# Performance work log

Measured on AMD Instinct MI355X. Metric: run time of the kernel, lower is better.

The kernel has to match this reference:

```python
import jax, jax.numpy as jnp
import numpy as np
from jax.ops import segment_sum

N_NODES = 100000
N_EDGES = 1600000
N_GRAPHS = 128
HIDDEN = 128
N_CLASSES = 10


def setup_inputs() -> dict:
    key = jax.random.key(0)
    ks = jax.random.split(key, 8)
    src = jax.random.randint(ks[0], (N_EDGES,), 0, N_NODES, dtype=jnp.int32)
    dst = jax.random.randint(ks[1], (N_EDGES,), 0, N_NODES, dtype=jnp.int32)
    graph_ids = jnp.sort(jax.random.randint(ks[2], (N_NODES,), 0, N_GRAPHS, dtype=jnp.int32))
    W1 = jax.random.normal(ks[3], (1, HIDDEN), dtype=jnp.float32)
    b1 = jnp.zeros((HIDDEN,), jnp.float32)
    W2 = jax.random.normal(ks[4], (HIDDEN, HIDDEN), dtype=jnp.float32) * 0.05
    b2 = jnp.zeros((HIDDEN,), jnp.float32)
    Wc = jax.random.normal(ks[5], (HIDDEN, N_CLASSES), dtype=jnp.float32) * 0.05
    bc = jnp.zeros((N_CLASSES,), jnp.float32)
    return {"src": src, "dst": dst, "graph_ids": graph_ids,
            "W1": W1, "b1": b1, "W2": W2, "b2": b2, "Wc": Wc, "bc": bc}


def _graph_conv(h, src, dst, norm_src, norm_dst, W, b, n_nodes):
    # DGL GraphConv, norm='both': D_out^{-1/2} gather -> scatter-sum -> W -> D_in^{-1/2} -> +b
    hs = h * norm_src[:, None]
    agg = segment_sum(hs[src], dst, num_segments=n_nodes)  # [N, F_in]
    return agg @ W * norm_dst[:, None] + b


def reference(src, dst, graph_ids, W1, b1, W2, b2, Wc, bc):
    n_nodes = graph_ids.shape[0]
    ones_e = jnp.ones(src.shape[0], jnp.float32)
    indeg = segment_sum(ones_e, dst, num_segments=n_nodes)
    outdeg = segment_sum(ones_e, src, num_segments=n_nodes)
    norm_src = jnp.clip(outdeg, 1.0, None) ** -0.5
    norm_dst = jnp.clip(indeg, 1.0, None) ** -0.5

    h = indeg[:, None]  # node feature = in-degree, [N, 1]
    h = jax.nn.relu(_graph_conv(h, src, dst, norm_src, norm_dst, W1, b1, n_nodes))
    h = jax.nn.relu(_graph_conv(h, src, dst, norm_src, norm_dst, W2, b2, n_nodes))

    # dgl.mean_nodes: per-graph mean pooling
    sums = segment_sum(h, graph_ids, num_segments=N_GRAPHS)          # [G, H]
    cnts = segment_sum(jnp.ones(n_nodes, jnp.float32), graph_ids, num_segments=N_GRAPHS)
    hg = sums / jnp.clip(cnts, 1.0, None)[:, None]
    return hg @ Wc + bc  # [G, n_classes]
```

## Files before the change

kernel.cpp:

```cpp
#include <hip/hip_runtime.h>

#define N_NODES   100000
#define N_EDGES   1600000
#define N_GRAPHS  128
#define HIDDEN    128
#define N_CLASSES 10

#define BSH   9
#define BSZ   512
#define NBUCK 196
#define CAP   16384
#define PCH   4096
#define PTH   512
#define PIT   (PCH / PTH)

typedef unsigned int   uint;
typedef unsigned short ushort;
typedef unsigned char  uchar;

__global__ __launch_bounds__(PTH)
void k_part(const int* __restrict__ src, const int* __restrict__ dst,
            unsigned* __restrict__ bcur1, unsigned* __restrict__ bcur2,
            unsigned* __restrict__ tmp1, ushort* __restrict__ tmp2, int nE) {
    __shared__ unsigned hist[256], scanT[256], lcur[256], base[256];
    __shared__ unsigned stag4[PCH];
    __shared__ uchar    stagB[PCH];
    int t = threadIdx.x;
    int e0 = blockIdx.x * PCH;
    int e1 = min(e0 + PCH, nE);
    int cntE = e1 - e0;

    int sv[PIT], dv[PIT];
    if (t < 256) hist[t] = 0;
    __syncthreads();
    #pragma unroll
    for (int m = 0; m < PIT; ++m) {
        int e = e0 + t + m * PTH;
        if (e < e1) {
            sv[m] = src[e]; dv[m] = dst[e];
            atomicAdd(&hist[dv[m] >> BSH], 1u);
        }
    }
    __syncthreads();
    unsigned v = (t < 256) ? hist[t] : 0u;
    if (t < 256) scanT[t] = v;
    __syncthreads();
    for (int off = 1; off < 256; off <<= 1) {
        unsigned add = (t < 256 && t >= off) ? scanT[t - off] : 0u;
        __syncthreads();
        if (t < 256) scanT[t] += add;
        __syncthreads();
    }
    if (t < 256) {
        unsigned excl = scanT[t] - v;
        lcur[t] = excl;
        if (v > 0) { unsigned g = atomicAdd(&bcur1[t], v); base[t] = (unsigned)t * CAP + g - excl; }
    }
    __syncthreads();
    #pragma unroll
    for (int m = 0; m < PIT; ++m) {
        int e = e0 + t + m * PTH;
        if (e < e1) {
            int d = dv[m], s = sv[m];
            int b = d >> BSH;
            unsigned p = atomicAdd(&lcur[b], 1u);
            stag4[p] = ((unsigned)(d & (BSZ - 1)) << 17) | (unsigned)s;
            stagB[p] = (uchar)b;
        }
    }
    __syncthreads();
    for (int i = t; i < cntE; i += PTH) {
        unsigned b = stagB[i];
        unsigned a = base[b] + (unsigned)i;
        if (a < (b + 1u) * CAP) tmp1[a] = stag4[i];
    }
    __syncthreads();

    if (t < 256) hist[t] = 0;
    __syncthreads();
    #pragma unroll
    for (int m = 0; m < PIT; ++m) {
        int e = e0 + t + m * PTH;
        if (e < e1) atomicAdd(&hist[sv[m] >> BSH], 1u);
    }
    __syncthreads();
    v = (t < 256) ? hist[t] : 0u;
    if (t < 256) scanT[t] = v;
    __syncthreads();
    for (int off = 1; off < 256; off <<= 1) {
        unsigned add = (t < 256 && t >= off) ? scanT[t - off] : 0u;
        __syncthreads();
        if (t < 256) scanT[t] += add;
        __syncthreads();
    }
    if (t < 256) {
        unsigned excl = scanT[t] - v;
        lcur[t] = excl;
        if (v > 0) { unsigned g = atomicAdd(&bcur2[t], v); base[t] = (unsigned)t * CAP + g - excl; }
    }
    __syncthreads();
    ushort* st2 = (ushort*)stag4;
    #pragma unroll
    for (int m = 0; m < PIT; ++m) {
        int e = e0 + t + m * PTH;
        if (e < e1) {
            int s = sv[m];
            int b = s >> BSH;
            unsigned p = atomicAdd(&lcur[b], 1u);
            st2[p]   = (ushort)(s & (BSZ - 1));
            stagB[p] = (uchar)b;
        }
    }
    __syncthreads();
    for (int i = t; i < cntE; i += PTH) {
        unsigned b = stagB[i];
        unsigned a = base[b] + (unsigned)i;
        if (a < (b + 1u) * CAP) tmp2[a] = st2[i];
    }
}

__global__ __launch_bounds__(1024)
void k_ind_csr(const unsigned* __restrict__ bcur1, const unsigned* __restrict__ tmp1,
               const unsigned* __restrict__ bcur2, const ushort* __restrict__ tmp2,
               unsigned* __restrict__ indeg, float* __restrict__ ns,
               float* __restrict__ hs0, int* __restrict__ rs,
               int* __restrict__ csr) {
    __shared__ unsigned cin[BSZ], cout[BSZ], pref[BSZ], lcur[BSZ];
    int b = blockIdx.x, t = threadIdx.x;
    if (t < BSZ) { cin[t] = 0; cout[t] = 0; }
    __syncthreads();
    unsigned f1 = min(bcur1[b], (unsigned)CAP);
    const unsigned* tp1 = tmp1 + (size_t)b * CAP;
    for (unsigned i = t; i < f1; i += 1024) atomicAdd(&cin[tp1[i] >> 17], 1u);
    unsigned f2 = min(bcur2[b], (unsigned)CAP);
    const ushort* tp2 = tmp2 + (size_t)b * CAP;
    for (unsigned i = t; i < f2; i += 1024) atomicAdd(&cout[tp2[i]], 1u);
    __syncthreads();
    unsigned v = (t < BSZ) ? cin[t] : 0u;
    if (t < BSZ) pref[t] = v;
    __syncthreads();
    for (int off = 1; off < BSZ; off <<= 1) {
        unsigned add = (t < BSZ && t >= off) ? pref[t - off] : 0u;
        __syncthreads();
        if (t < BSZ) pref[t] += add;
        __syncthreads();
    }
    if (t < BSZ) {
        unsigned excl = pref[t] - v;
        lcur[t] = excl;
        int n = b * BSZ + t;
        if (n < N_NODES) {
            unsigned ci = cin[t], co = cout[t];
            float nsv = rsqrtf(fmaxf((float)co, 1.0f));
            indeg[n] = ci;
            ns[n]    = nsv;
            hs0[n]   = (float)ci * nsv;
            rs[n]    = (int)(b * CAP + excl);
        }
    }
    __syncthreads();
    int* cb = csr + (size_t)b * CAP;
    for (unsigned i = t; i < f1; i += 1024) {
        unsigned e = tp1[i];
        unsigned pos = atomicAdd(&lcur[e >> 17], 1u);
        cb[pos] = (int)(e & 0x1FFFFu);
    }
}

__global__ __launch_bounds__(256)
void k_conv1_info(const int* __restrict__ rs, const int* __restrict__ csr,
                  const float* __restrict__ hs0, const unsigned* __restrict__ indeg,
                  const float* __restrict__ ns,
                  const float* __restrict__ W1, const float* __restrict__ b1,
                  const float* __restrict__ W2,
                  float* __restrict__ U, float* __restrict__ V,
                  float4* __restrict__ info, int nN) {
    __shared__ float sts[128];
    int t = threadIdx.x;
    if (t < 128) {
        float w = W1[t], bb = b1[t];
        sts[t] = (w != 0.0f) ? (-bb / w) : 1e30f;
    }
    __syncthreads();
    for (int k = 2; k <= 128; k <<= 1) {
        for (int j = k >> 1; j > 0; j >>= 1) {
            if (t < 128) {
                int ixj = t ^ j;
                if (ixj > t) {
                    float a = sts[t], bb = sts[ixj];
                    bool up = ((t & k) == 0);
                    if (up ? (a > bb) : (a < bb)) { sts[t] = bb; sts[ixj] = a; }
                }
            }
            __syncthreads();
        }
    }
    if (blockIdx.x < 129 && t < 128) {
        int sg = blockIdx.x;
        float a_rep;
        if (sg == 0)        a_rep = sts[0]   - 1.0f;
        else if (sg == 128) a_rep = sts[127] + 1.0f;
        else                a_rep = 0.5f * (sts[sg - 1] + sts[sg]);
        float u = 0.0f, vv = 0.0f;
        for (int j = 0; j < 128; ++j) {
            float w = W1[j], bb = b1[j];
            if (a_rep * w + bb > 0.0f) {
                float w2 = W2[j * HIDDEN + t];
                u  += w * w2;
                vv += bb * w2;
            }
        }
        U[sg * HIDDEN + t] = u;
        V[sg * HIDDEN + t] = vv;
    }
    int node = blockIdx.x * 128 + (t >> 1);
    if (node >= nN) return;
    int j  = t & 1;
    int r0 = rs[node];
    int c  = (int)indeg[node];
    float a = 0.0f;
    #pragma unroll 4
    for (int k = j; k < c; k += 2) a += hs0[csr[r0 + k]];
    a += __shfl_xor(a, 1);
    float nd = rsqrtf(fmaxf((float)c, 1.0f));
    float av = a * nd;
    int sgp = 0;
    #pragma unroll
    for (int q = 0; q < 64; ++q) sgp += (sts[2 * q + j] < av) ? 1 : 0;
    sgp += __shfl_xor(sgp, 1);
    if (j == 0) {
        float nsv = ns[node];
        info[node] = make_float4(nsv * av, nsv, __int_as_float(sgp), nd);
    }
}

__global__ __launch_bounds__(256)
void k_conv2_pool(const int* __restrict__ rs, const int* __restrict__ csr,
                  const float4* __restrict__ info, const unsigned* __restrict__ indeg,
                  const float* __restrict__ U, const float* __restrict__ V,
                  const int* __restrict__ graph_ids, const float* __restrict__ b2,
                  float* __restrict__ pool, float* __restrict__ cnt, int nN) {
    __shared__ float sA[64], sB[64], sND[64];
    __shared__ int   sSg[64], sGr[64], sR[64], sC[64];
    int blockBase = blockIdx.x * 64;
    int t = threadIdx.x;
    int node = blockBase + (t >> 2);
    int j = t & 3;

    float A = 0.0f, B = 0.0f;
    int mn = 255, mx = 0;
    int r0 = 0, c = 0;
    if (node < nN) {
        r0 = rs[node]; c = (int)indeg[node];
        #pragma unroll 4
        for (int k = j; k < c; k += 4) {
            float4 nf = info[csr[r0 + k]];
            int sg = __float_as_int(nf.z);
            A += nf.x; B += nf.y;
            mn = min(mn, sg); mx = max(mx, sg);
        }
    }
    A += __shfl_xor(A, 1); A += __shfl_xor(A, 2);
    B += __shfl_xor(B, 1); B += __shfl_xor(B, 2);
    mn = min(mn, __shfl_xor(mn, 1)); mn = min(mn, __shfl_xor(mn, 2));
    mx = max(mx, __shfl_xor(mx, 1)); mx = max(mx, __shfl_xor(mx, 2));
    if (node < nN && j == 0) {
        int i = t >> 2;
        sA[i] = A; sB[i] = B;
        sSg[i] = (mn << 8) | mx;
        sR[i] = r0; sC[i] = c;
        sND[i] = info[node].w;
        sGr[i] = graph_ids[node];
    }
    __syncthreads();
    if (t >= 64) return;
    int lane = t;

    float bb0 = b2[lane], bb1 = b2[64 + lane];
    int gcur = -1;
    float racc0 = 0.0f, racc1 = 0.0f, cl = 0.0f;

    for (int i = 0; i < 64; ++i) {
        int n = blockBase + i;
        if (n >= nN) break;
        int pk = sSg[i], smn = pk >> 8, smx = pk & 255;
        float acc0, acc1;
        if (smn >= smx) {
            int sg = min(smn, 128);
            float Av = sA[i], Bv = sB[i];
            const float* Ur = U + sg * HIDDEN;
            const float* Vr = V + sg * HIDDEN;
            acc0 = Av * Ur[lane]      + Bv * Vr[lane];
            acc1 = Av * Ur[64 + lane] + Bv * Vr[64 + lane];
        } else {
            acc0 = 0.0f; acc1 = 0.0f;
            int rr = sR[i], cc = sC[i];
            for (int k = 0; k < cc; ++k) {
                float4 nf = info[csr[rr + k]];
                int sg = __float_as_int(nf.z);
                const float* Ur = U + sg * HIDDEN;
                const float* Vr = V + sg * HIDDEN;
                acc0 += nf.x * Ur[lane]      + nf.y * Vr[lane];
                acc1 += nf.x * Ur[64 + lane] + nf.y * Vr[64 + lane];
            }
        }
        float nd = sND[i];
        float r0v = fmaxf(nd * acc0 + bb0, 0.0f);
        float r1v = fmaxf(nd * acc1 + bb1, 0.0f);
        int g = sGr[i];
        if (g != gcur) {
            if (gcur >= 0) {
                atomicAdd(&pool[gcur * HIDDEN + lane],      racc0);
                atomicAdd(&pool[gcur * HIDDEN + 64 + lane], racc1);
                if (lane == 0) atomicAdd(&cnt[gcur], cl);
            }
            gcur = g; racc0 = 0.0f; racc1 = 0.0f; cl = 0.0f;
        }
        racc0 += r0v; racc1 += r1v; cl += 1.0f;
    }
    if (gcur >= 0) {
        atomicAdd(&pool[gcur * HIDDEN + lane],      racc0);
        atomicAdd(&pool[gcur * HIDDEN + 64 + lane], racc1);
        if (lane == 0) atomicAdd(&cnt[gcur], cl);
    }
}

__global__ void k_final(const float* __restrict__ pool, const float* __restrict__ cnt,
                        const float* __restrict__ Wc, const float* __restrict__ bc,
                        float* __restrict__ out) {
    int t = blockIdx.x * blockDim.x + threadIdx.x;
    if (t >= N_GRAPHS * N_CLASSES) return;
    int g = t / N_CLASSES, c = t % N_CLASSES;
    float inv = 1.0f / fmaxf(cnt[g], 1.0f);
    float acc = bc[c];
    for (int j = 0; j < HIDDEN; ++j)
        acc += pool[g * HIDDEN + j] * inv * Wc[j * N_CLASSES + c];
    out[t] = acc;
}

extern "C" void kernel_launch(void* const* d_in, const int* in_sizes, int n_in,
                              void* d_out, int out_size, void* d_ws, size_t ws_size,
                              hipStream_t stream) {
    const int*   src       = (const int*)d_in[0];
    const int*   dst       = (const int*)d_in[1];
    const int*   graph_ids = (const int*)d_in[2];
    const float* W1        = (const float*)d_in[3];
    const float* b1        = (const float*)d_in[4];
    const float* W2        = (const float*)d_in[5];
    const float* b2        = (const float*)d_in[6];
    const float* Wc        = (const float*)d_in[7];
    const float* bc        = (const float*)d_in[8];
    float* out = (float*)d_out;

    char* ws = (char*)d_ws;
    size_t off = 0;
    auto alloc = [&](size_t elems) { void* p = ws + off; off += elems * 4; return p; };

    unsigned* bcur1 = (unsigned*)alloc(256);
    unsigned* bcur2 = (unsigned*)alloc(256);
    float*    pool  = (float*)   alloc(N_GRAPHS * HIDDEN);
    float*    cnt   = (float*)   alloc(N_GRAPHS);
    size_t zero_bytes = off;
    float4*   info  = (float4*)  alloc((size_t)N_NODES * 4);
    unsigned* tmp1  = (unsigned*)alloc((size_t)NBUCK * CAP);
    ushort*   tmp2  = (ushort*)  alloc((size_t)NBUCK * CAP / 2);
    int*      csr   = (int*)     alloc((size_t)NBUCK * CAP);
    int*      rs    = (int*)     alloc(N_NODES);
    unsigned* indeg = (unsigned*)alloc(N_NODES);
    float*    nsA   = (float*)   alloc(N_NODES);
    float*    hs0   = (float*)   alloc(N_NODES);
    float*    U     = (float*)   alloc(129 * HIDDEN);
    float*    V     = (float*)   alloc(129 * HIDDEN);

    hipMemsetAsync(d_ws, 0, zero_bytes, stream);

    int pblocks  = (N_EDGES + PCH - 1) / PCH;
    int c1blocks = (N_NODES + 127) / 128;
    int c2blocks = (N_NODES + 63) / 64;
    k_part      <<<pblocks, PTH, 0, stream>>>(src, dst, bcur1, bcur2, tmp1, tmp2, N_EDGES);
    k_ind_csr   <<<NBUCK, 1024, 0, stream>>>(bcur1, tmp1, bcur2, tmp2, indeg, nsA, hs0, rs, csr);
    k_conv1_info<<<c1blocks, 256, 0, stream>>>(rs, csr, hs0, indeg, nsA, W1, b1, W2, U, V, info, N_NODES);
    k_conv2_pool<<<c2blocks, 256, 0, stream>>>(rs, csr, info, indeg, U, V, graph_ids, b2, pool, cnt, N_NODES);
    k_final     <<<(N_GRAPHS * N_CLASSES + 255) / 256, 256, 0, stream>>>(pool, cnt, Wc, bc, out);
}
```

Before: 183.2 us.

## Fuse all five stages into one cooperative persistent kernel with grid syncs

Replaces the five separate kernel launches with a single cooperative kernel of 512 blocks that runs partitioning, CSR build, conv1, conv2+pooling and the classifier as phases separated by grid.sync(). Work per phase is redistributed across the fixed grid: each block handles a contiguous slab of edges or nodes, and the pooling phase splits each block's nodes across its eight waves. This removes launch gaps and inter-kernel drain, at the cost of grid-wide barriers, lower per-phase parallelism in some stages (e.g. only 196 blocks active during CSR build), and reloading src/dst from global memory instead of holding them in registers.

```diff
diff --git a/kernel.cpp b/kernel.cpp
--- a/kernel.cpp
+++ b/kernel.cpp
@@ -1,4 +1,7 @@
 #include <hip/hip_runtime.h>
+#include <hip/hip_cooperative_groups.h>
+
+namespace cg = cooperative_groups;
 
 #define N_NODES   100000
 #define N_EDGES   1600000
@@ -10,176 +13,170 @@
 #define BSZ   512
 #define NBUCK 196
 #define CAP   16384
-#define PCH   4096
-#define PTH   512
-#define PIT   (PCH / PTH)
+#define GRID  512
+#define BLK   512
+#define EPB   (N_EDGES / GRID)
+#define SMAX  3200
+#define NPB   ((N_NODES + GRID - 1) / GRID)
 
 typedef unsigned int   uint;
 typedef unsigned short ushort;
 typedef unsigned char  uchar;
 
-__global__ __launch_bounds__(PTH)
-void k_part(const int* __restrict__ src, const int* __restrict__ dst,
-            unsigned* __restrict__ bcur1, unsigned* __restrict__ bcur2,
-            unsigned* __restrict__ tmp1, ushort* __restrict__ tmp2, int nE) {
-    __shared__ unsigned hist[256], scanT[256], lcur[256], base[256];
-    __shared__ unsigned stag4[PCH];
-    __shared__ uchar    stagB[PCH];
-    int t = threadIdx.x;
-    int e0 = blockIdx.x * PCH;
-    int e1 = min(e0 + PCH, nE);
+union ShMem {
+    struct {
+        unsigned hist[256], scanT[256], lcur[256], base[256];
+        unsigned stag[SMAX];
+        uchar    stagB[SMAX];
+    } p1;
+    struct {
+        unsigned cin[BSZ], cout[BSZ], pref[BSZ], lcur[BSZ];
+    } p2;
+    struct { float sts[128]; } p3;
+    struct {
+        float sA[256], sB[256], sND[256];
+        int   sSg[256], sGr[256], sR[256], sC[256];
+    } p4;
+};
+
+__global__ __launch_bounds__(BLK, 4)
+void k_fused(const int* __restrict__ src, const int* __restrict__ dst,
+             const int* __restrict__ graph_ids,
+             const float* __restrict__ W1, const float* __restrict__ b1,
+             const float* __restrict__ W2, const float* __restrict__ b2,
+             const float* __restrict__ Wc, const float* __restrict__ bc,
+             float* __restrict__ out,
+             unsigned* bcur1, unsigned* bcur2,
+             unsigned* tmp1, ushort* tmp2, int* csr, int* rs,
+             unsigned* indeg, float* nsA, float* hs0,
+             float* U, float* V, float4* info,
+             float* pool, float* cnt)
+{
+    cg::grid_group grid = cg::this_grid();
+    __shared__ ShMem sh;
+    int t = threadIdx.x, blk = blockIdx.x;
+
+    int e0 = blk * EPB, e1 = min(e0 + EPB, N_EDGES);
     int cntE = e1 - e0;
-
-    int sv[PIT], dv[PIT];
-    if (t < 256) hist[t] = 0;
-    __syncthreads();
-    #pragma unroll
-    for (int m = 0; m < PIT; ++m) {
-        int e = e0 + t + m * PTH;
-        if (e < e1) {
-            sv[m] = src[e]; dv[m] = dst[e];
-            atomicAdd(&hist[dv[m] >> BSH], 1u);
-        }
-    }
-    __syncthreads();
-    unsigned v = (t < 256) ? hist[t] : 0u;
-    if (t < 256) scanT[t] = v;
-    __syncthreads();
-    for (int off = 1; off < 256; off <<= 1) {
-        unsigned add = (t < 256 && t >= off) ? scanT[t - off] : 0u;
-        __syncthreads();
-        if (t < 256) scanT[t] += add;
-        __syncthreads();
-    }
-    if (t < 256) {
-        unsigned excl = scanT[t] - v;
-        lcur[t] = excl;
-        if (v > 0) { unsigned g = atomicAdd(&bcur1[t], v); base[t] = (unsigned)t * CAP + g - excl; }
-    }
-    __syncthreads();
-    #pragma unroll
-    for (int m = 0; m < PIT; ++m) {
-        int e = e0 + t + m * PTH;
-        if (e < e1) {
-            int d = dv[m], s = sv[m];
-            int b = d >> BSH;
-            unsigned p = atomicAdd(&lcur[b], 1u);
-            stag4[p] = ((unsigned)(d & (BSZ - 1)) << 17) | (unsigned)s;
-            stagB[p] = (uchar)b;
-        }
-    }
-    __syncthreads();
-    for (int i = t; i < cntE; i += PTH) {
-        unsigned b = stagB[i];
-        unsigned a = base[b] + (unsigned)i;
-        if (a < (b + 1u) * CAP) tmp1[a] = stag4[i];
-    }
-    __syncthreads();
-
-    if (t < 256) hist[t] = 0;
-    __syncthreads();
-    #pragma unroll
-    for (int m = 0; m < PIT; ++m) {
-        int e = e0 + t + m * PTH;
-        if (e < e1) atomicAdd(&hist[sv[m] >> BSH], 1u);
-    }
-    __syncthreads();
-    v = (t < 256) ? hist[t] : 0u;
-    if (t < 256) scanT[t] = v;
-    __syncthreads();
-    for (int off = 1; off < 256; off <<= 1) {
-        unsigned add = (t < 256 && t >= off) ? scanT[t - off] : 0u;
-        __syncthreads();
-        if (t < 256) scanT[t] += add;
-        __syncthreads();
-    }
-    if (t < 256) {
-        unsigned excl = scanT[t] - v;
-        lcur[t] = excl;
-        if (v > 0) { unsigned g = atomicAdd(&bcur2[t], v); base[t] = (unsigned)t * CAP + g - excl; }
-    }
-    __syncthreads();
-    ushort* st2 = (ushort*)stag4;
-    #pragma unroll
-    for (int m = 0; m < PIT; ++m) {
-        int e = e0 + t + m * PTH;
-        if (e < e1) {
-            int s = sv[m];
+    if (t < 256) sh.p1.hist[t] = 0;
+    __syncthreads();
+    for (int e = e0 + t; e < e1; e += BLK)
+        atomicAdd(&sh.p1.hist[dst[e] >> BSH], 1u);
+    __syncthreads();
+    {
+        unsigned v = (t < 256) ? sh.p1.hist[t] : 0u;
+        if (t < 256) sh.p1.scanT[t] = v;
+        __syncthreads();
+        for (int off = 1; off < 256; off <<= 1) {
+            unsigned add = (t < 256 && t >= off) ? sh.p1.scanT[t - off] : 0u;
+            __syncthreads();
+            if (t < 256) sh.p1.scanT[t] += add;
+            __syncthreads();
+        }
+        if (t < 256) {
+            unsigned excl = sh.p1.scanT[t] - v;
+            sh.p1.lcur[t] = excl;
+            if (v) { unsigned g = atomicAdd(&bcur1[t], v); sh.p1.base[t] = (unsigned)t * CAP + g - excl; }
+        }
+    }
+    __syncthreads();
+    for (int e = e0 + t; e < e1; e += BLK) {
+        int d = dst[e], s = src[e];
+        int b = d >> BSH;
+        unsigned p = atomicAdd(&sh.p1.lcur[b], 1u);
+        sh.p1.stag[p]  = ((unsigned)(d & (BSZ - 1)) << 17) | (unsigned)s;
+        sh.p1.stagB[p] = (uchar)b;
+    }
+    __syncthreads();
+    for (int i = t; i < cntE; i += BLK) {
+        unsigned b = sh.p1.stagB[i];
+        unsigned a = sh.p1.base[b] + (unsigned)i;
+        if (a < (b + 1u) * CAP) tmp1[a] = sh.p1.stag[i];
+    }
+    __syncthreads();
+    if (t < 256) sh.p1.hist[t] = 0;
+    __syncthreads();
+    for (int e = e0 + t; e < e1; e += BLK)
+        atomicAdd(&sh.p1.hist[src[e] >> BSH], 1u);
+    __syncthreads();
+    {
+        unsigned v = (t < 256) ? sh.p1.hist[t] : 0u;
+        if (t < 256) sh.p1.scanT[t] = v;
+        __syncthreads();
+        for (int off = 1; off < 256; off <<= 1) {
+            unsigned add = (t < 256 && t >= off) ? sh.p1.scanT[t - off] : 0u;
+            __syncthreads();
+            if (t < 256) sh.p1.scanT[t] += add;
+            __syncthreads();
+        }
+        if (t < 256) {
+            unsigned excl = sh.p1.scanT[t] - v;
+            sh.p1.lcur[t] = excl;
+            if (v) { unsigned g = atomicAdd(&bcur2[t], v); sh.p1.base[t] = (unsigned)t * CAP + g - excl; }
+        }
+    }
+    __syncthreads();
+    {
+        ushort* st2 = (ushort*)sh.p1.stag;
+        for (int e = e0 + t; e < e1; e += BLK) {
+            int s = src[e];
             int b = s >> BSH;
-            unsigned p = atomicAdd(&lcur[b], 1u);
-            st2[p]   = (ushort)(s & (BSZ - 1));
-            stagB[p] = (uchar)b;
-        }
-    }
-    __syncthreads();
-    for (int i = t; i < cntE; i += PTH) {
-        unsigned b = stagB[i];
-        unsigned a = base[b] + (unsigned)i;
-        if (a < (b + 1u) * CAP) tmp2[a] = st2[i];
-    }
-}
-
-__global__ __launch_bounds__(1024)
-void k_ind_csr(const unsigned* __restrict__ bcur1, const unsigned* __restrict__ tmp1,
-               const unsigned* __restrict__ bcur2, const ushort* __restrict__ tmp2,
-               unsigned* __restrict__ indeg, float* __restrict__ ns,
-               float* __restrict__ hs0, int* __restrict__ rs,
-               int* __restrict__ csr) {
-    __shared__ unsigned cin[BSZ], cout[BSZ], pref[BSZ], lcur[BSZ];
-    int b = blockIdx.x, t = threadIdx.x;
-    if (t < BSZ) { cin[t] = 0; cout[t] = 0; }
-    __syncthreads();
-    unsigned f1 = min(bcur1[b], (unsigned)CAP);
-    const unsigned* tp1 = tmp1 + (size_t)b * CAP;
-    for (unsigned i = t; i < f1; i += 1024) atomicAdd(&cin[tp1[i] >> 17], 1u);
-    unsigned f2 = min(bcur2[b], (unsigned)CAP);
-    const ushort* tp2 = tmp2 + (size_t)b * CAP;
-    for (unsigned i = t; i < f2; i += 1024) atomicAdd(&cout[tp2[i]], 1u);
-    __syncthreads();
-    unsigned v = (t < BSZ) ? cin[t] : 0u;
-    if (t < BSZ) pref[t] = v;
-    __syncthreads();
-    for (int off = 1; off < BSZ; off <<= 1) {
-        unsigned add = (t < BSZ && t >= off) ? pref[t - off] : 0u;
-        __syncthreads();
-        if (t < BSZ) pref[t] += add;
-        __syncthreads();
-    }
-    if (t < BSZ) {
-        unsigned excl = pref[t] - v;
-        lcur[t] = excl;
-        int n = b * BSZ + t;
+            unsigned p = atomicAdd(&sh.p1.lcur[b], 1u);
+            st2[p]         = (ushort)(s & (BSZ - 1));
+            sh.p1.stagB[p] = (uchar)b;
+        }
+        __syncthreads();
+        for (int i = t; i < cntE; i += BLK) {
+            unsigned b = sh.p1.stagB[i];
+            unsigned a = sh.p1.base[b] + (unsigned)i;
+            if (a < (b + 1u) * CAP) tmp2[a] = st2[i];
+        }
+    }
+    grid.sync();
+
+    if (blk < NBUCK) {
+        sh.p2.cin[t] = 0; sh.p2.cout[t] = 0;
+        __syncthreads();
+        unsigned f1 = min(bcur1[blk], (unsigned)CAP);
+        const unsigned* tp1 = tmp1 + (size_t)blk * CAP;
+        for (unsigned i = t; i < f1; i += BLK) atomicAdd(&sh.p2.cin[tp1[i] >> 17], 1u);
+        unsigned f2 = min(bcur2[blk], (unsigned)CAP);
+        const ushort* tp2 = tmp2 + (size_t)blk * CAP;
+        for (unsigned i = t; i < f2; i += BLK) atomicAdd(&sh.p2.cout[tp2[i]], 1u);
+        __syncthreads();
+        unsigned v = sh.p2.cin[t];
+        sh.p2.pref[t] = v;
+        __syncthreads();
+        for (int off = 1; off < BSZ; off <<= 1) {
+            unsigned add = (t >= off) ? sh.p2.pref[t - off] : 0u;
+            __syncthreads();
+            sh.p2.pref[t] += add;
+            __syncthreads();
+        }
+        unsigned excl = sh.p2.pref[t] - v;
+        sh.p2.lcur[t] = excl;
+        int n = blk * BSZ + t;
         if (n < N_NODES) {
-            unsigned ci = cin[t], co = cout[t];
+            unsigned co = sh.p2.cout[t];
             float nsv = rsqrtf(fmaxf((float)co, 1.0f));
-            indeg[n] = ci;
-            ns[n]    = nsv;
-            hs0[n]   = (float)ci * nsv;
-            rs[n]    = (int)(b * CAP + excl);
-        }
-    }
-    __syncthreads();
-    int* cb = csr + (size_t)b * CAP;
-    for (unsigned i = t; i < f1; i += 1024) {
-        unsigned e = tp1[i];
-        unsigned pos = atomicAdd(&lcur[e >> 17], 1u);
-        cb[pos] = (int)(e & 0x1FFFFu);
-    }
-}
-
-__global__ __launch_bounds__(256)
-void k_conv1_info(const int* __restrict__ rs, const int* __restrict__ csr,
-                  const float* __restrict__ hs0, const unsigned* __restrict__ indeg,
-                  const float* __restrict__ ns,
-                  const float* __restrict__ W1, const float* __restrict__ b1,
-                  const float* __restrict__ W2,
-                  float* __restrict__ U, float* __restrict__ V,
-                  float4* __restrict__ info, int nN) {
-    __shared__ float sts[128];
-    int t = threadIdx.x;
+            indeg[n] = v;
+            nsA[n]   = nsv;
+            hs0[n]   = (float)v * nsv;
+            rs[n]    = (int)(blk * CAP + excl);
+        }
+        __syncthreads();
+        int* cb = csr + (size_t)blk * CAP;
+        for (unsigned i = t; i < f1; i += BLK) {
+            unsigned e = tp1[i];
+            unsigned pos = atomicAdd(&sh.p2.lcur[e >> 17], 1u);
+            cb[pos] = (int)(e & 0x1FFFFu);
+        }
+    }
+    grid.sync();
+
     if (t < 128) {
         float w = W1[t], bb = b1[t];
-        sts[t] = (w != 0.0f) ? (-bb / w) : 1e30f;
+        sh.p3.sts[t] = (w != 0.0f) ? (-bb / w) : 1e30f;
     }
     __syncthreads();
     for (int k = 2; k <= 128; k <<= 1) {
@@ -187,20 +184,20 @@
             if (t < 128) {
                 int ixj = t ^ j;
                 if (ixj > t) {
-                    float a = sts[t], bb = sts[ixj];
+                    float a = sh.p3.sts[t], bb = sh.p3.sts[ixj];
                     bool up = ((t & k) == 0);
-                    if (up ? (a > bb) : (a < bb)) { sts[t] = bb; sts[ixj] = a; }
+                    if (up ? (a > bb) : (a < bb)) { sh.p3.sts[t] = bb; sh.p3.sts[ixj] = a; }
                 }
             }
             __syncthreads();
         }
     }
-    if (blockIdx.x < 129 && t < 128) {
-        int sg = blockIdx.x;
+    if (blk < 129 && t < 128) {
+        int sg = blk;
         float a_rep;
-        if (sg == 0)        a_rep = sts[0]   - 1.0f;
-        else if (sg == 128) a_rep = sts[127] + 1.0f;
-        else                a_rep = 0.5f * (sts[sg - 1] + sts[sg]);
+        if (sg == 0)        a_rep = sh.p3.sts[0]   - 1.0f;
+        else if (sg == 128) a_rep = sh.p3.sts[127] + 1.0f;
+        else                a_rep = 0.5f * (sh.p3.sts[sg - 1] + sh.p3.sts[sg]);
         float u = 0.0f, vv = 0.0f;
         for (int j = 0; j < 128; ++j) {
             float w = W1[j], bb = b1[j];
@@ -213,129 +210,124 @@
         U[sg * HIDDEN + t] = u;
         V[sg * HIDDEN + t] = vv;
     }
-    int node = blockIdx.x * 128 + (t >> 1);
-    if (node >= nN) return;
-    int j  = t & 1;
-    int r0 = rs[node];
-    int c  = (int)indeg[node];
-    float a = 0.0f;
-    #pragma unroll 4
-    for (int k = j; k < c; k += 2) a += hs0[csr[r0 + k]];
-    a += __shfl_xor(a, 1);
-    float nd = rsqrtf(fmaxf((float)c, 1.0f));
-    float av = a * nd;
-    int sgp = 0;
-    #pragma unroll
-    for (int q = 0; q < 64; ++q) sgp += (sts[2 * q + j] < av) ? 1 : 0;
-    sgp += __shfl_xor(sgp, 1);
-    if (j == 0) {
-        float nsv = ns[node];
-        info[node] = make_float4(nsv * av, nsv, __int_as_float(sgp), nd);
-    }
-}
-
-__global__ __launch_bounds__(256)
-void k_conv2_pool(const int* __restrict__ rs, const int* __restrict__ csr,
-                  const float4* __restrict__ info, const unsigned* __restrict__ indeg,
-                  const float* __restrict__ U, const float* __restrict__ V,
-                  const int* __restrict__ graph_ids, const float* __restrict__ b2,
-                  float* __restrict__ pool, float* __restrict__ cnt, int nN) {
-    __shared__ float sA[64], sB[64], sND[64];
-    __shared__ int   sSg[64], sGr[64], sR[64], sC[64];
-    int blockBase = blockIdx.x * 64;
-    int t = threadIdx.x;
-    int node = blockBase + (t >> 2);
-    int j = t & 3;
-
-    float A = 0.0f, B = 0.0f;
-    int mn = 255, mx = 0;
-    int r0 = 0, c = 0;
-    if (node < nN) {
-        r0 = rs[node]; c = (int)indeg[node];
-        #pragma unroll 4
-        for (int k = j; k < c; k += 4) {
-            float4 nf = info[csr[r0 + k]];
-            int sg = __float_as_int(nf.z);
-            A += nf.x; B += nf.y;
-            mn = min(mn, sg); mx = max(mx, sg);
-        }
-    }
-    A += __shfl_xor(A, 1); A += __shfl_xor(A, 2);
-    B += __shfl_xor(B, 1); B += __shfl_xor(B, 2);
-    mn = min(mn, __shfl_xor(mn, 1)); mn = min(mn, __shfl_xor(mn, 2));
-    mx = max(mx, __shfl_xor(mx, 1)); mx = max(mx, __shfl_xor(mx, 2));
-    if (node < nN && j == 0) {
-        int i = t >> 2;
-        sA[i] = A; sB[i] = B;
-        sSg[i] = (mn << 8) | mx;
-        sR[i] = r0; sC[i] = c;
-        sND[i] = info[node].w;
-        sGr[i] = graph_ids[node];
-    }
-    __syncthreads();
-    if (t >= 64) return;
-    int lane = t;
-
-    float bb0 = b2[lane], bb1 = b2[64 + lane];
-    int gcur = -1;
-    float racc0 = 0.0f, racc1 = 0.0f, cl = 0.0f;
-
-    for (int i = 0; i < 64; ++i) {
-        int n = blockBase + i;
-        if (n >= nN) break;
-        int pk = sSg[i], smn = pk >> 8, smx = pk & 255;
-        float acc0, acc1;
-        if (smn >= smx) {
-            int sg = min(smn, 128);
-            float Av = sA[i], Bv = sB[i];
-            const float* Ur = U + sg * HIDDEN;
-            const float* Vr = V + sg * HIDDEN;
-            acc0 = Av * Ur[lane]      + Bv * Vr[lane];
-            acc1 = Av * Ur[64 + lane] + Bv * Vr[64 + lane];
-        } else {
-            acc0 = 0.0f; acc1 = 0.0f;
-            int rr = sR[i], cc = sC[i];
-            for (int k = 0; k < cc; ++k) {
-                float4 nf = info[csr[rr + k]];
+    {
+        int node = blk * NPB + (t >> 1);
+        if (t < 2 * NPB && node < N_NODES) {
+            int j  = t & 1;
+            int r0 = rs[node];
+            int c  = (int)indeg[node];
+            float a = 0.0f;
+            #pragma unroll 4
+            for (int k = j; k < c; k += 2) a += hs0[csr[r0 + k]];
+            a += __shfl_xor(a, 1);
+            float nd = rsqrtf(fmaxf((float)c, 1.0f));
+            float av = a * nd;
+            int sgp = 0;
+            #pragma unroll
+            for (int q = 0; q < 64; ++q) sgp += (sh.p3.sts[2 * q + j] < av) ? 1 : 0;
+            sgp += __shfl_xor(sgp, 1);
+            if (j == 0) {
+                float nsv = nsA[node];
+                info[node] = make_float4(nsv * av, nsv, __int_as_float(sgp), nd);
+            }
+        }
+    }
+    grid.sync();
+
+    int base4 = blk * NPB;
+    for (int p = 0; p < 2; ++p) {
+        int li = p * 128 + (t >> 2);
+        int node = base4 + li;
+        int j = t & 3;
+        float A = 0.0f, B = 0.0f;
+        int mn = 255, mx = 0, r0 = 0, c = 0;
+        bool act = (li < NPB) && (node < N_NODES);
+        if (act) {
+            r0 = rs[node]; c = (int)indeg[node];
+            #pragma unroll 4
+            for (int k = j; k < c; k += 4) {
+                float4 nf = info[csr[r0 + k]];
                 int sg = __float_as_int(nf.z);
+                A += nf.x; B += nf.y;
+                mn = min(mn, sg); mx = max(mx, sg);
+            }
+        }
+        A += __shfl_xor(A, 1); A += __shfl_xor(A, 2);
+        B += __shfl_xor(B, 1); B += __shfl_xor(B, 2);
+        mn = min(mn, __shfl_xor(mn, 1)); mn = min(mn, __shfl_xor(mn, 2));
+        mx = max(mx, __shfl_xor(mx, 1)); mx = max(mx, __shfl_xor(mx, 2));
+        if (act && j == 0) {
+            sh.p4.sA[li] = A; sh.p4.sB[li] = B;
+            sh.p4.sSg[li] = (mn << 8) | mx;
+            sh.p4.sR[li] = r0; sh.p4.sC[li] = c;
+            sh.p4.sND[li] = info[node].w;
+            sh.p4.sGr[li] = graph_ids[node];
+        }
+    }
+    __syncthreads();
+    {
+        int w = t >> 6, lane = t & 63;
+        int li0 = w * 25, li1 = min(li0 + 25, NPB);
+        float bb0 = b2[lane], bb1 = b2[64 + lane];
+        int gcur = -1;
+        float racc0 = 0.0f, racc1 = 0.0f, cl = 0.0f;
+        for (int li = li0; li < li1; ++li) {
+            int node = base4 + li;
+            if (node >= N_NODES) break;
+            int pk = sh.p4.sSg[li], smn = pk >> 8, smx = pk & 255;
+            float acc0, acc1;
+            if (smn >= smx) {
+                int sg = min(smn, 128);
+                float Av = sh.p4.sA[li], Bv = sh.p4.sB[li];
                 const float* Ur = U + sg * HIDDEN;
                 const float* Vr = V + sg * HIDDEN;
-                acc0 += nf.x * Ur[lane]      + nf.y * Vr[lane];
-                acc1 += nf.x * Ur[64 + lane] + nf.y * Vr[64 + lane];
-            }
-        }
-        float nd = sND[i];
-        float r0v = fmaxf(nd * acc0 + bb0, 0.0f);
-        float r1v = fmaxf(nd * acc1 + bb1, 0.0f);
-        int g = sGr[i];
-        if (g != gcur) {
-            if (gcur >= 0) {
-                atomicAdd(&pool[gcur * HIDDEN + lane],      racc0);
-                atomicAdd(&pool[gcur * HIDDEN + 64 + lane], racc1);
-                if (lane == 0) atomicAdd(&cnt[gcur], cl);
-            }
-            gcur = g; racc0 = 0.0f; racc1 = 0.0f; cl = 0.0f;
-        }
-        racc0 += r0v; racc1 += r1v; cl += 1.0f;
-    }
-    if (gcur >= 0) {
-        atomicAdd(&pool[gcur * HIDDEN + lane],      racc0);
-        atomicAdd(&pool[gcur * HIDDEN + 64 + lane], racc1);
-        if (lane == 0) atomicAdd(&cnt[gcur], cl);
-    }
-}
-
-__global__ void k_final(const float* __restrict__ pool, const float* __restrict__ cnt,
-                        const float* __restrict__ Wc, const float* __restrict__ bc,
-                        float* __restrict__ out) {
-    int t = blockIdx.x * blockDim.x + threadIdx.x;
-    if (t >= N_GRAPHS * N_CLASSES) return;
-    int g = t / N_CLASSES, c = t % N_CLASSES;
-    float inv = 1.0f / fmaxf(cnt[g], 1.0f);
-    float acc = bc[c];
-    for (int j = 0; j < HIDDEN; ++j)
-        acc += pool[g * HIDDEN + j] * inv * Wc[j * N_CLASSES + c];
-    out[t] = acc;
+                acc0 = Av * Ur[lane]      + Bv * Vr[lane];
+                acc1 = Av * Ur[64 + lane] + Bv * Vr[64 + lane];
+            } else {
+                acc0 = 0.0f; acc1 = 0.0f;
+                int rr = sh.p4.sR[li], cc = sh.p4.sC[li];
+                for (int k = 0; k < cc; ++k) {
+                    float4 nf = info[csr[rr + k]];
+                    int sg = __float_as_int(nf.z);
+                    const float* Ur = U + sg * HIDDEN;
+                    const float* Vr = V + sg * HIDDEN;
+                    acc0 += nf.x * Ur[lane]      + nf.y * Vr[lane];
+                    acc1 += nf.x * Ur[64 + lane] + nf.y * Vr[64 + lane];
+                }
+            }
+            float nd = sh.p4.sND[li];
+            float r0v = fmaxf(nd * acc0 + bb0, 0.0f);
+            float r1v = fmaxf(nd * acc1 + bb1, 0.0f);
+            int g = sh.p4.sGr[li];
+            if (g != gcur) {
+                if (gcur >= 0) {
+                    atomicAdd(&pool[gcur * HIDDEN + lane],      racc0);
+                    atomicAdd(&pool[gcur * HIDDEN + 64 + lane], racc1);
+                    if (lane == 0) atomicAdd(&cnt[gcur], cl);
+                }
+                gcur = g; racc0 = 0.0f; racc1 = 0.0f; cl = 0.0f;
+            }
+            racc0 += r0v; racc1 += r1v; cl += 1.0f;
+        }
+        if (gcur >= 0) {
+            atomicAdd(&pool[gcur * HIDDEN + lane],      racc0);
+            atomicAdd(&pool[gcur * HIDDEN + 64 + lane], racc1);
+            if (lane == 0) atomicAdd(&cnt[gcur], cl);
+        }
+    }
+    grid.sync();
+
+    if (blk < 5 && t < 256) {
+        int idx = blk * 256 + t;
+        if (idx < N_GRAPHS * N_CLASSES) {
+            int g = idx / N_CLASSES, c = idx % N_CLASSES;
+            float inv = 1.0f / fmaxf(cnt[g], 1.0f);
+            float acc = bc[c];
+            for (int j = 0; j < HIDDEN; ++j)
+                acc += pool[g * HIDDEN + j] * inv * Wc[j * N_CLASSES + c];
+            out[idx] = acc;
+        }
+    }
 }
 
 extern "C" void kernel_launch(void* const* d_in, const int* in_sizes, int n_in,
@@ -374,12 +366,15 @@
 
     hipMemsetAsync(d_ws, 0, zero_bytes, stream);
 
-    int pblocks  = (N_EDGES + PCH - 1) / PCH;
-    int c1blocks = (N_NODES + 127) / 128;
-    int c2blocks = (N_NODES + 63) / 64;
-    k_part      <<<pblocks, PTH, 0, stream>>>(src, dst, bcur1, bcur2, tmp1, tmp2, N_EDGES);
-    k_ind_csr   <<<NBUCK, 1024, 0, stream>>>(bcur1, tmp1, bcur2, tmp2, indeg, nsA, hs0, rs, csr);
-    k_conv1_info<<<c1blocks, 256, 0, stream>>>(rs, csr, hs0, indeg, nsA, W1, b1, W2, U, V, info, N_NODES);
-    k_conv2_pool<<<c2blocks, 256, 0, stream>>>(rs, csr, info, indeg, U, V, graph_ids, b2, pool, cnt, N_NODES);
-    k_final     <<<(N_GRAPHS * N_CLASSES + 255) / 256, 256, 0, stream>>>(pool, cnt, Wc, bc, out);
+    void* args[] = {
+        (void*)&src, (void*)&dst, (void*)&graph_ids,
+        (void*)&W1, (void*)&b1, (void*)&W2, (void*)&b2,
+        (void*)&Wc, (void*)&bc, (void*)&out,
+        (void*)&bcur1, (void*)&bcur2,
+        (void*)&tmp1, (void*)&tmp2, (void*)&csr, (void*)&rs,
+        (void*)&indeg, (void*)&nsA, (void*)&hs0,
+        (void*)&U, (void*)&V, (void*)&info,
+        (void*)&pool, (void*)&cnt
+    };
+    hipLaunchCooperativeKernel((void*)k_fused, dim3(GRID), dim3(BLK), args, 0, stream);
 }
```

Result: slower. 428.1 us (+133.7%).
